# Kernel optimization log

Measured on AMD Instinct MI355X. Metric: run time of the kernel, lower is better.

The kernel has to match this reference:

```python
import jax, jax.numpy as jnp
import numpy as np

B, T, F, H, OUT = 256, 256, 128, 1024, 128


def setup_inputs() -> dict:
    key = jax.random.key(0)
    ks = jax.random.split(key, 6)
    s_ih = 1.0 / np.sqrt(H)
    return {
        "x": jax.random.normal(ks[0], (B, T, F), dtype=jnp.float32),
        "h0": jnp.zeros((B, H), dtype=jnp.float32),
        "c0": jnp.zeros((B, H), dtype=jnp.float32),
        "W_ih": jax.random.normal(ks[1], (4 * H, F), dtype=jnp.float32) * s_ih,
        "W_hh": jax.random.normal(ks[2], (4 * H, H), dtype=jnp.float32) * s_ih,
        "b_ih": jax.random.normal(ks[3], (4 * H,), dtype=jnp.float32) * s_ih,
        "b_hh": jax.random.normal(ks[4], (4 * H,), dtype=jnp.float32) * s_ih,
        "W_fc": jax.random.normal(ks[5], (OUT, H), dtype=jnp.float32) * s_ih,
        "b_fc": jnp.zeros((OUT,), dtype=jnp.float32),
    }


def _lstm_scan(x, h0, c0, W_ih, W_hh, b_ih, b_hh):
    # Precompute input projections for all timesteps: [T, B, 4H]
    x_t = jnp.swapaxes(x, 0, 1)  # [T, B, F]
    x_proj = jnp.einsum('tbf,gf->tbg', x_t, W_ih) + b_ih + b_hh

    def step(carry, xp):
        h, c = carry
        gates = xp + h @ W_hh.T  # [B, 4H]
        i, f, g, o = jnp.split(gates, 4, axis=-1)  # PyTorch LSTMCell gate order
        i = jax.nn.sigmoid(i)
        f = jax.nn.sigmoid(f)
        g = jnp.tanh(g)
        o = jax.nn.sigmoid(o)
        c = f * c + i * g
        h = o * jnp.tanh(c)
        return (h, c), None

    (h, c), _ = jax.lax.scan(step, (h0, c0), x_proj)
    return h, c


def reference(x, h0, c0, W_ih, W_hh, b_ih, b_hh, W_fc, b_fc):
    h, c = _lstm_scan(x, h0, c0, W_ih, W_hh, b_ih, b_hh)
    sig_out = jax.nn.sigmoid(h)
    # Dropout is identity in eval/reference mode
    return sig_out @ W_fc.T + b_fc  # [B, OUT]
```

## Files before the change

kernel.cpp:

```cpp
#include <hip/hip_runtime.h>


typedef _Float16 f16x8 __attribute__((ext_vector_type(8)));
typedef float f32x16 __attribute__((ext_vector_type(16)));
typedef unsigned long long u64;

#define SCOPE_AGENT __HIP_MEMORY_SCOPE_AGENT

#define WS_WP    0ull
#define WS_BIAS  9437184ull
#define WS_XT    (WS_BIAS + 16384ull)
#define WS_HB0   (WS_XT + 16777216ull)
#define WS_HB1   (WS_HB0 + 524288ull)
#define WS_SIGH  (WS_HB1 + 524288ull)
#define WS_BAR   (WS_SIGH + 1048576ull)

__device__ __forceinline__ unsigned short f2h(float f) {
  _Float16 h = (_Float16)f;
  return __builtin_bit_cast(unsigned short, h);
}

__device__ __forceinline__ float fast_sig(float x) {
  return __builtin_amdgcn_rcpf(1.f + __expf(-x));
}
__device__ __forceinline__ float fast_tanh(float x) {
  return __builtin_fmaf(2.f, fast_sig(2.f * x), -1.f);
}

__global__ void prep_pack(const float* __restrict__ W_ih, const float* __restrict__ W_hh,
                          const float* __restrict__ b_ih, const float* __restrict__ b_hh,
                          unsigned short* __restrict__ wp, float* __restrict__ bias) {
  unsigned i = blockIdx.x * 256u + threadIdx.x;
  if (i < 4718592u) {
    unsigned j = i & 7u;
    unsigned l = (i >> 3) & 63u;
    unsigned rest = i >> 9;
    unsigned q = rest % 18u;
    unsigned rest2 = rest / 18u;
    unsigned n = rest2 & 3u;
    unsigned rest3 = rest2 >> 2;
    unsigned w = rest3 & 3u;
    unsigned cg = rest3 >> 2;
    unsigned gcol = n * 1024u + cg * 32u + (l & 31u);
    unsigned khi = (l >> 5) * 8u + j;
    float v;
    if (q < 16u) {
      unsigned k = w * 256u + q * 16u + khi;
      v = W_hh[(size_t)gcol * 1024u + k];
    } else {
      unsigned k = w * 32u + (q - 16u) * 16u + khi;
      v = W_ih[(size_t)gcol * 128u + k];
    }
    wp[i] = f2h(v);
  }
  if (i < 4096u) bias[i] = b_ih[i] + b_hh[i];
}

__global__ void prep_misc(const float* __restrict__ x, const float* __restrict__ h0,
                          unsigned short* __restrict__ xT, unsigned short* __restrict__ hb0,
                          unsigned* __restrict__ bar) {
  unsigned i = blockIdx.x * 256u + threadIdx.x;
  if (i < 8388608u) {
    unsigned f = i & 127u;
    unsigned b = (i >> 7) & 255u;
    unsigned t = i >> 15;
    xT[i] = f2h(x[((size_t)b * 256u + t) * 128u + f]);
  }
  if (i < 262144u) hb0[i] = f2h(h0[i]);
  if (i < 768u) bar[i] = 0u;
}

__launch_bounds__(256, 1)
__global__ void lstm_main(const unsigned short* __restrict__ wp,
                          const float* __restrict__ bias,
                          const unsigned short* __restrict__ xT,
                          unsigned short* __restrict__ hb0,
                          unsigned short* __restrict__ hb1,
                          const float* __restrict__ c0,
                          float* __restrict__ sigh,
                          unsigned* __restrict__ bar) {
  extern __shared__ char lds[];
  float4* redv = (float4*)lds;
  unsigned short* hst = (unsigned short*)(lds + 65536);

  const unsigned tid = threadIdx.x;
  const unsigned wg  = blockIdx.x;
  const unsigned w   = tid >> 6;
  const unsigned l   = tid & 63u;
  const unsigned rg  = wg >> 5;
  const unsigned cg  = wg & 31u;
  const unsigned lo5 = l & 31u;
  const unsigned hi  = l >> 5;

  int4 Braw[4][18];
  {
    const int4* wpv = (const int4*)wp;
    const unsigned wbase = (cg * 4u + w) * 4608u;
#pragma unroll
    for (int n = 0; n < 4; ++n) {
#pragma unroll
      for (int q = 0; q < 18; ++q) {
        Braw[n][q] = wpv[wbase + (unsigned)(n * 18 + q) * 64u + l];
      }
    }
  }

  float bias_v[4];
#pragma unroll
  for (int n = 0; n < 4; ++n) bias_v[n] = bias[(unsigned)n * 1024u + cg * 32u + lo5];

  const unsigned col = cg * 32u + lo5;
  float c_st[4];
  unsigned soff[4];
#pragma unroll
  for (int i = 0; i < 4; ++i) {
    unsigned r = rg * 32u + 8u * w + (unsigned)i + 4u * hi;
    soff[i] = r * 1024u + col;
    c_st[i] = c0[soff[i]];
  }

  const unsigned fbase = lo5 * 2048u + w * 512u + hi * 16u;
  const unsigned fxor  = (lo5 & 7u) << 4;

  const unsigned sg16 = tid * 16u;
  unsigned xb = ((rg * 32u + lo5) * 128u + w * 32u + hi * 8u) * 2u;

  const char* hrd = (const char*)hb0;
  char* hwr = (char*)hb1;
  const char* xbase = (const char*)xT;
  unsigned* flags = &bar[rg * 32u];
  const unsigned tilebase = rg * 65536u;

  const unsigned srow = tid >> 3;
  const unsigned sseg = tid & 7u;
  const unsigned sgoff = (((rg * 32u + srow) * 1024u) + cg * 32u + sseg * 4u) * 2u;

  int4 xr[2];
  xr[0] = *(const int4*)(xbase + xb);
  xr[1] = *(const int4*)(xbase + xb + 32u);

  for (unsigned t = 0; t < 256u; ++t) {
    u64 sa[16], sb[16];
#pragma unroll
    for (int r = 0; r < 16; ++r) {
      const char* src = hrd + tilebase + (unsigned)r * 4096u + sg16;
      sa[r] = __hip_atomic_load((const u64*)src,       __ATOMIC_RELAXED, SCOPE_AGENT);
      sb[r] = __hip_atomic_load((const u64*)(src + 8), __ATOMIC_RELAXED, SCOPE_AGENT);
    }

    f32x16 acc[4] = {};
#pragma unroll
    for (int qx = 0; qx < 2; ++qx) {
      f16x8 a = __builtin_bit_cast(f16x8, xr[qx]);
      acc[0] = __builtin_amdgcn_mfma_f32_32x32x16_f16(a, __builtin_bit_cast(f16x8, Braw[0][16 + qx]), acc[0], 0, 0, 0);
      acc[1] = __builtin_amdgcn_mfma_f32_32x32x16_f16(a, __builtin_bit_cast(f16x8, Braw[1][16 + qx]), acc[1], 0, 0, 0);
      acc[2] = __builtin_amdgcn_mfma_f32_32x32x16_f16(a, __builtin_bit_cast(f16x8, Braw[2][16 + qx]), acc[2], 0, 0, 0);
      acc[3] = __builtin_amdgcn_mfma_f32_32x32x16_f16(a, __builtin_bit_cast(f16x8, Braw[3][16 + qx]), acc[3], 0, 0, 0);
    }

#pragma unroll
    for (int r = 0; r < 16; ++r) {
      unsigned d = (unsigned)r * 4096u + sg16;
      unsigned a = d ^ (((d >> 11) & 7u) << 4);
      *(u64*)(lds + a)     = sa[r];
      *(u64*)(lds + a + 8) = sb[r];
    }
    __syncthreads();

#pragma unroll
    for (int q = 0; q < 16; ++q) {
      int4 av = *(const int4*)(lds + ((fbase + (unsigned)q * 32u) ^ fxor));
      f16x8 a = __builtin_bit_cast(f16x8, av);
      acc[0] = __builtin_amdgcn_mfma_f32_32x32x16_f16(a, __builtin_bit_cast(f16x8, Braw[0][q]), acc[0], 0, 0, 0);
      acc[1] = __builtin_amdgcn_mfma_f32_32x32x16_f16(a, __builtin_bit_cast(f16x8, Braw[1][q]), acc[1], 0, 0, 0);
      acc[2] = __builtin_amdgcn_mfma_f32_32x32x16_f16(a, __builtin_bit_cast(f16x8, Braw[2][q]), acc[2], 0, 0, 0);
      acc[3] = __builtin_amdgcn_mfma_f32_32x32x16_f16(a, __builtin_bit_cast(f16x8, Braw[3][q]), acc[3], 0, 0, 0);
    }
    __syncthreads();

#pragma unroll
    for (int n = 0; n < 4; ++n) {
#pragma unroll
      for (int c = 0; c < 4; ++c) {
        float4 v;
        v.x = acc[n][4 * c + 0]; v.y = acc[n][4 * c + 1];
        v.z = acc[n][4 * c + 2]; v.w = acc[n][4 * c + 3];
        redv[((w * 4u + (unsigned)n) * 4u + (unsigned)c) * 64u + l] = v;
      }
    }
    __syncthreads();

    float gv[4][4];
#pragma unroll
    for (int n = 0; n < 4; ++n) {
      float4 s; s.x = bias_v[n]; s.y = bias_v[n]; s.z = bias_v[n]; s.w = bias_v[n];
#pragma unroll
      for (int wo = 0; wo < 4; ++wo) {
        float4 v = redv[(((unsigned)wo * 4u + (unsigned)n) * 4u + w) * 64u + l];
        s.x += v.x; s.y += v.y; s.z += v.z; s.w += v.w;
      }
      gv[n][0] = s.x; gv[n][1] = s.y; gv[n][2] = s.z; gv[n][3] = s.w;
    }

    const bool last = (t == 255u);
#pragma unroll
    for (int i = 0; i < 4; ++i) {
      float ig = fast_sig(gv[0][i]);
      float fg = fast_sig(gv[1][i]);
      float gg = fast_tanh(gv[2][i]);
      float og = fast_sig(gv[3][i]);
      float cc = fg * c_st[i] + ig * gg;
      c_st[i] = cc;
      float hh = og * fast_tanh(cc);
      hst[(8u * w + (unsigned)i + 4u * hi) * 32u + lo5] = f2h(hh);
      if (last) sigh[soff[i]] = fast_sig(hh);
    }

    if (!last) {
      __syncthreads();
      {
        u64 v = *(const u64*)(hst + srow * 32u + sseg * 4u);
        __hip_atomic_store((u64*)(hwr + sgoff), v, __ATOMIC_RELAXED, SCOPE_AGENT);
      }
      xb += 65536u;
      xr[0] = *(const int4*)(xbase + xb);
      xr[1] = *(const int4*)(xbase + xb + 32u);
      __syncthreads();
      if (tid == 0)
        __hip_atomic_store(&flags[cg], t + 1u, __ATOMIC_RELAXED, SCOPE_AGENT);
      if (tid < 64u) {
        const unsigned tgt = t + 1u;
        for (;;) {
          unsigned f = __hip_atomic_load(&flags[l & 31u], __ATOMIC_RELAXED, SCOPE_AGENT);
          if (__all(f >= tgt)) break;
          __builtin_amdgcn_s_sleep(1);
        }
      }
      __syncthreads();
    }

    const char* tmp = hrd; hrd = hwr; hwr = (char*)tmp;
  }
}

__global__ void final_fc(const float* __restrict__ sigh, const float* __restrict__ W_fc,
                         const float* __restrict__ b_fc, float* __restrict__ out) {
  unsigned b = blockIdx.x;
  unsigned o = threadIdx.x;
  const float* hrow = sigh + (size_t)b * 1024u;
  const float* wrow = W_fc + (size_t)o * 1024u;
  float acc = b_fc[o];
#pragma unroll 8
  for (unsigned k = 0; k < 1024u; k += 4u) {
    float4 hv = *(const float4*)(hrow + k);
    float4 wv = *(const float4*)(wrow + k);
    acc += hv.x * wv.x + hv.y * wv.y + hv.z * wv.z + hv.w * wv.w;
  }
  out[b * 128u + o] = acc;
}

extern "C" void kernel_launch(void* const* d_in, const int* in_sizes, int n_in,
                              void* d_out, int out_size, void* d_ws, size_t ws_size,
                              hipStream_t stream) {
  (void)in_sizes; (void)n_in; (void)out_size; (void)ws_size;
  const float* x    = (const float*)d_in[0];
  const float* h0   = (const float*)d_in[1];
  const float* c0   = (const float*)d_in[2];
  const float* W_ih = (const float*)d_in[3];
  const float* W_hh = (const float*)d_in[4];
  const float* b_ih = (const float*)d_in[5];
  const float* b_hh = (const float*)d_in[6];
  const float* W_fc = (const float*)d_in[7];
  const float* b_fc = (const float*)d_in[8];

  char* ws = (char*)d_ws;
  unsigned short* wp   = (unsigned short*)(ws + WS_WP);
  float*          bias = (float*)(ws + WS_BIAS);
  unsigned short* xT   = (unsigned short*)(ws + WS_XT);
  unsigned short* hb0  = (unsigned short*)(ws + WS_HB0);
  unsigned short* hb1  = (unsigned short*)(ws + WS_HB1);
  float*          sigh = (float*)(ws + WS_SIGH);
  unsigned*       bar  = (unsigned*)(ws + WS_BAR);
  float*          out  = (float*)d_out;

  prep_pack<<<18432, 256, 0, stream>>>(W_ih, W_hh, b_ih, b_hh, wp, bias);
  prep_misc<<<32768, 256, 0, stream>>>(x, h0, xT, hb0, bar);
  lstm_main<<<256, 256, 67584, stream>>>(wp, bias, xT, hb0, hb1, c0, sigh, bar);
  final_fc<<<256, 128, 0, stream>>>(sigh, W_fc, b_fc, out);
}
```

Baseline: 1.314 ms.

## Give each wave a private LDS h-tile and quad-buffer h to drop block barriers

Each wave now stages its own slice of the hidden state into a private LDS region, so the block-wide barriers around the h staging and MFMA phase become a local lgkmcnt wait. The reduction buffer moves to a separate LDS region, and h uses four global buffers indexed by t mod 4 instead of ping-pong. Every wave polls a subset of the inter-block flags itself, which removes the trailing __syncthreads after the spin-wait. The intent is to cut intra-block synchronisation per timestep. The cost is doubled LDS use (133 KB) and more subtle cross-block ordering that relies on the deeper buffering.

Measured after the change: 1.307 ms. About the same (-0.5%).

```diff
diff --git a/kernel.cpp b/kernel.cpp
--- a/kernel.cpp
+++ b/kernel.cpp
@@ -10,9 +10,8 @@
 #define WS_WP    0ull
 #define WS_BIAS  9437184ull
 #define WS_XT    (WS_BIAS + 16384ull)
-#define WS_HB0   (WS_XT + 16777216ull)
-#define WS_HB1   (WS_HB0 + 524288ull)
-#define WS_SIGH  (WS_HB1 + 524288ull)
+#define WS_HB    (WS_XT + 16777216ull)
+#define WS_SIGH  (WS_HB + 4ull * 524288ull)
 #define WS_BAR   (WS_SIGH + 1048576ull)
 
 __device__ __forceinline__ unsigned short f2h(float f) {
@@ -74,14 +73,13 @@
 __global__ void lstm_main(const unsigned short* __restrict__ wp,
                           const float* __restrict__ bias,
                           const unsigned short* __restrict__ xT,
-                          unsigned short* __restrict__ hb0,
-                          unsigned short* __restrict__ hb1,
+                          unsigned short* __restrict__ hb,
                           const float* __restrict__ c0,
                           float* __restrict__ sigh,
                           unsigned* __restrict__ bar) {
   extern __shared__ char lds[];
-  float4* redv = (float4*)lds;
-  unsigned short* hst = (unsigned short*)(lds + 65536);
+  float4* redv = (float4*)(lds + 65536);
+  unsigned short* hst = (unsigned short*)(lds + 131072);
 
   const unsigned tid = threadIdx.x;
   const unsigned wg  = blockIdx.x;
@@ -119,17 +117,16 @@
     c_st[i] = c0[soff[i]];
   }
 
-  const unsigned fbase = lo5 * 2048u + w * 512u + hi * 16u;
+  const unsigned sgsrc0 = (rg * 32u + hi) * 2048u + w * 512u + lo5 * 16u;
+  const unsigned sdst0  = w * 16384u + hi * 512u + lo5 * 16u;
+  const unsigned fbase = w * 16384u + lo5 * 512u + hi * 16u;
   const unsigned fxor  = (lo5 & 7u) << 4;
 
-  const unsigned sg16 = tid * 16u;
   unsigned xb = ((rg * 32u + lo5) * 128u + w * 32u + hi * 8u) * 2u;
 
-  const char* hrd = (const char*)hb0;
-  char* hwr = (char*)hb1;
   const char* xbase = (const char*)xT;
+  const char* hbase = (const char*)hb;
   unsigned* flags = &bar[rg * 32u];
-  const unsigned tilebase = rg * 65536u;
 
   const unsigned srow = tid >> 3;
   const unsigned sseg = tid & 7u;
@@ -140,10 +137,13 @@
   xr[1] = *(const int4*)(xbase + xb + 32u);
 
   for (unsigned t = 0; t < 256u; ++t) {
+    const char* hrd = hbase + ((t & 3u) * 524288u);
+    char* hwr = (char*)hbase + (((t + 1u) & 3u) * 524288u);
+
     u64 sa[16], sb[16];
 #pragma unroll
     for (int r = 0; r < 16; ++r) {
-      const char* src = hrd + tilebase + (unsigned)r * 4096u + sg16;
+      const char* src = hrd + sgsrc0 + (unsigned)r * 4096u;
       sa[r] = __hip_atomic_load((const u64*)src,       __ATOMIC_RELAXED, SCOPE_AGENT);
       sb[r] = __hip_atomic_load((const u64*)(src + 8), __ATOMIC_RELAXED, SCOPE_AGENT);
     }
@@ -160,12 +160,12 @@
 
 #pragma unroll
     for (int r = 0; r < 16; ++r) {
-      unsigned d = (unsigned)r * 4096u + sg16;
-      unsigned a = d ^ (((d >> 11) & 7u) << 4);
-      *(u64*)(lds + a)     = sa[r];
-      *(u64*)(lds + a + 8) = sb[r];
-    }
-    __syncthreads();
+      unsigned d = sdst0 + (unsigned)r * 1024u;
+      unsigned a = d ^ (((d >> 9) & 7u) << 4);
+      struct { u64 a, b; } p = { sa[r], sb[r] };
+      *(int4*)(lds + a) = __builtin_bit_cast(int4, p);
+    }
+    asm volatile("s_waitcnt lgkmcnt(0)" ::: "memory");
 
 #pragma unroll
     for (int q = 0; q < 16; ++q) {
@@ -176,7 +176,6 @@
       acc[2] = __builtin_amdgcn_mfma_f32_32x32x16_f16(a, __builtin_bit_cast(f16x8, Braw[2][q]), acc[2], 0, 0, 0);
       acc[3] = __builtin_amdgcn_mfma_f32_32x32x16_f16(a, __builtin_bit_cast(f16x8, Braw[3][q]), acc[3], 0, 0, 0);
     }
-    __syncthreads();
 
 #pragma unroll
     for (int n = 0; n < 4; ++n) {
@@ -228,18 +227,16 @@
       __syncthreads();
       if (tid == 0)
         __hip_atomic_store(&flags[cg], t + 1u, __ATOMIC_RELAXED, SCOPE_AGENT);
-      if (tid < 64u) {
+      {
         const unsigned tgt = t + 1u;
+        const unsigned fidx = w * 8u + (l & 7u);
         for (;;) {
-          unsigned f = __hip_atomic_load(&flags[l & 31u], __ATOMIC_RELAXED, SCOPE_AGENT);
-          if (__all(f >= tgt)) break;
+          unsigned f = __hip_atomic_load(&flags[fidx], __ATOMIC_RELAXED, SCOPE_AGENT);
+          if (__all(l >= 8u || f >= tgt)) break;
           __builtin_amdgcn_s_sleep(1);
         }
       }
-      __syncthreads();
-    }
-
-    const char* tmp = hrd; hrd = hwr; hwr = (char*)tmp;
+    }
   }
 }
 
@@ -277,14 +274,13 @@
   unsigned short* wp   = (unsigned short*)(ws + WS_WP);
   float*          bias = (float*)(ws + WS_BIAS);
   unsigned short* xT   = (unsigned short*)(ws + WS_XT);
-  unsigned short* hb0  = (unsigned short*)(ws + WS_HB0);
-  unsigned short* hb1  = (unsigned short*)(ws + WS_HB1);
+  unsigned short* hb   = (unsigned short*)(ws + WS_HB);
   float*          sigh = (float*)(ws + WS_SIGH);
   unsigned*       bar  = (unsigned*)(ws + WS_BAR);
   float*          out  = (float*)d_out;
 
   prep_pack<<<18432, 256, 0, stream>>>(W_ih, W_hh, b_ih, b_hh, wp, bias);
-  prep_misc<<<32768, 256, 0, stream>>>(x, h0, xT, hb0, bar);
-  lstm_main<<<256, 256, 67584, stream>>>(wp, bias, xT, hb0, hb1, c0, sigh, bar);
+  prep_misc<<<32768, 256, 0, stream>>>(x, h0, xT, hb, bar);
+  lstm_main<<<256, 256, 133120, stream>>>(wp, bias, xT, hb, c0, sigh, bar);
   final_fc<<<256, 128, 0, stream>>>(sigh, W_fc, b_fc, out);
 }
```
